# Kernel tuning notes

Measured on AMD Instinct MI355X. Metric: run time of the kernel, lower is better.

The kernel has to match this reference:

```python
import jax, jax.numpy as jnp
import numpy as np

B, DIM, H, W = 4, 256, 64, 64
DSTATE, EXPAND, DCONV = 64, 2, 4
DINNER = EXPAND * DIM            # 512
HEADDIM = 64
NHEADS = DINNER // HEADDIM       # 8
DINPROJ = 2 * DINNER + 2 * DSTATE + NHEADS   # z, xBC, dt
CONVDIM = DINNER + 2 * DSTATE
EPS = 1e-5


def setup_inputs() -> dict:
    key = jax.random.key(0)
    ks = jax.random.split(key, 12)
    n = lambda i, shape, sc=1.0: jax.random.normal(ks[i], shape, jnp.float32) * sc
    return {
        "x": n(0, (B, DIM, H, W)),
        "Q1": n(1, (B, 1, H, W)),
        "Q2": n(2, (B, 1, H, W)),
        "S": jax.random.uniform(ks[3], (B, 1, H, W), jnp.float32),
        "ln_g": jnp.ones((DIM,), jnp.float32),
        "ln_b": jnp.zeros((DIM,), jnp.float32),
        "W_in": n(4, (DIM, DINPROJ), 0.02),
        "conv_w": n(5, (CONVDIM, DCONV), 0.2),
        "conv_b": jnp.zeros((CONVDIM,), jnp.float32),
        "dt_bias": n(6, (NHEADS,), 0.5),
        "A_log": jnp.log(jnp.linspace(1.0, 8.0, NHEADS)).astype(jnp.float32),
        "Dskip": n(7, (NHEADS,), 0.3) + 1.0,
        "norm_w": jnp.ones((DINNER,), jnp.float32),
        "W_out": n(8, (DINNER, DIM), 0.02),
        "gn_g": jnp.ones((DIM,), jnp.float32),
        "gn_b": jnp.zeros((DIM,), jnp.float32),
        "conv1_w": n(9, (DIM, DIM), 0.05),
    }


def _mamba(seq, W_in, conv_w, conv_b, dt_bias, A_log, Dskip, norm_w, W_out):
    # seq: (Ns, L, D) -- Mamba-2 style SSD forward
    Ns, L, _ = seq.shape
    zxbcdt = seq @ W_in                                   # (Ns,L,DINPROJ)
    z = zxbcdt[..., :DINNER]
    xBC = zxbcdt[..., DINNER:DINNER + CONVDIM]
    dt = zxbcdt[..., DINNER + CONVDIM:]                   # (Ns,L,nh)
    # causal depthwise conv (kernel DCONV) + silu
    xp = jnp.pad(xBC, ((0, 0), (DCONV - 1, 0), (0, 0)))
    xBC = sum(conv_w[:, k] * xp[:, k:k + L, :] for k in range(DCONV)) + conv_b
    xBC = jax.nn.silu(xBC)
    xh = xBC[..., :DINNER].reshape(Ns, L, NHEADS, HEADDIM)
    Bm = xBC[..., DINNER:DINNER + DSTATE]                 # (Ns,L,n) ngroups=1
    Cm = xBC[..., DINNER + DSTATE:]
    dt = jax.nn.softplus(dt + dt_bias)
    A = -jnp.exp(A_log)                                   # (nh,)
    dA = jnp.exp(dt * A)                                  # (Ns,L,nh)
    dBx = jnp.einsum('slh,slhp,sln->slhpn', dt, xh, Bm)   # (Ns,L,nh,hd,n)

    def step(h, inp):
        a, bx, c = inp
        h = a[:, :, None, None] * h + bx                  # (Ns,nh,hd,n)
        return h, jnp.einsum('shpn,sn->shp', h, c)

    h0 = jnp.zeros((Ns, NHEADS, HEADDIM, DSTATE), seq.dtype)
    _, ys = jax.lax.scan(step, h0, (dA.transpose(1, 0, 2),
                                    dBx.transpose(1, 0, 2, 3, 4),
                                    Cm.transpose(1, 0, 2)))
    y = ys.transpose(1, 0, 2, 3) + Dskip[None, None, :, None] * xh
    y = y.reshape(Ns, L, DINNER)
    y = y * jax.nn.silu(z)                                # gated RMSNorm
    y = y * jax.lax.rsqrt(jnp.mean(y * y, axis=-1, keepdims=True) + EPS) * norm_w
    return y @ W_out


def _scan_merge(xn, dim_scan, mp):
    Bb, C, Hh, Ww = xn.shape
    if dim_scan == 3:
        seq = xn.transpose(0, 2, 3, 1).reshape(Bb * Hh, Ww, C)
    else:
        seq = xn.transpose(0, 3, 2, 1).reshape(Bb * Ww, Hh, C)
    fwd = _mamba(seq, *mp)
    bwd = jnp.flip(_mamba(jnp.flip(seq, 1), *mp), 1)
    out = 0.5 * (fwd + bwd)
    if dim_scan == 3:
        return out.reshape(Bb, Hh, Ww, C).transpose(0, 3, 1, 2)
    return out.reshape(Bb, Ww, Hh, C).transpose(0, 3, 2, 1)


def reference(x, Q1, Q2, S, ln_g, ln_b, W_in, conv_w, conv_b, dt_bias, A_log,
              Dskip, norm_w, W_out, gn_g, gn_b, conv1_w):
    # LayerNorm over channel dim
    xt = x.transpose(0, 2, 3, 1)                          # (B,H,W,C)
    mu = xt.mean(-1, keepdims=True)
    var = ((xt - mu) ** 2).mean(-1, keepdims=True)
    xn = ((xt - mu) * jax.lax.rsqrt(var + EPS) * ln_g + ln_b).transpose(0, 3, 1, 2)
    mp = (W_in, conv_w, conv_b, dt_bias, A_log, Dskip, norm_w, W_out)
    f_H = _scan_merge(xn, 3, mp)                          # horizontal (along W)
    f_V = _scan_merge(xn, 2, mp)                          # vertical (along H)
    alpha = jax.nn.sigmoid(Q1)
    fg = (alpha * f_H + (1 - alpha) * f_V) * (0.5 + 0.5 * S)
    # out_proj: Conv1x1 (no bias) + GroupNorm(1) + GELU
    y = jnp.einsum('bchw,oc->bohw', fg, conv1_w)
    mu = y.mean((1, 2, 3), keepdims=True)
    var = ((y - mu) ** 2).mean((1, 2, 3), keepdims=True)
    y = (y - mu) * jax.lax.rsqrt(var + EPS) * gn_g[None, :, None, None] + gn_b[None, :, None, None]
    return jax.nn.gelu(y, approximate=False)
```

## Files before the change

kernel.cpp:

```cpp
#include <hip/hip_runtime.h>
#include <hip/hip_bf16.h>

#define EPSF 1e-5f

typedef unsigned short u16;
typedef __attribute__((ext_vector_type(8))) short short8;
typedef __attribute__((ext_vector_type(4))) float f32x4;

__device__ __forceinline__ float sigf(float x){ return 1.f/(1.f+__expf(-x)); }
__device__ __forceinline__ float siluf(float x){ return x/(1.f+__expf(-x)); }
__device__ __forceinline__ u16 f2bf(float x){ __hip_bfloat16 h = __float2bfloat16(x); return *reinterpret_cast<u16*>(&h); }
__device__ __forceinline__ float bf2f(u16 u){ __hip_bfloat16 h; *reinterpret_cast<u16*>(&h) = u; return __bfloat162float(h); }

union BF8 { short8 v; u16 h[8]; uint4 q; };

__device__ __forceinline__ short8 ldg_frag(const u16* p){
  BF8 u; u.q = *(const uint4*)p; return u.v;
}
#define MFMA16(a,b,c) __builtin_amdgcn_mfma_f32_16x16x32_bf16((a),(b),(c),0,0,0)

__global__ __launch_bounds__(256) void k_ln(const float* __restrict__ x,
                                            const float* __restrict__ g,
                                            const float* __restrict__ b,
                                            u16* __restrict__ xn){
  __shared__ float XL[256][65];
  __shared__ float red[2][4][64];
  __shared__ float muL[64], rsL[64];
  int blk = blockIdx.x; int bb = blk>>6, h = blk&63;
  int t = threadIdx.x;
  const float* xb = x + ((size_t)bb*256*4096) + h*64;
  for(int i=0;i<64;i++){ int idx = t + 256*i; int c = idx>>6, w = idx&63;
    XL[c][w] = xb[(size_t)c*4096 + w]; }
  __syncthreads();
  { int w = t & 63, q = t >> 6;
    float s1=0, s2=0;
    for(int c=q*64;c<q*64+64;c++){ float v = XL[c][w]; s1+=v; s2+=v*v; }
    red[0][q][w]=s1; red[1][q][w]=s2; }
  __syncthreads();
  if(t<64){ float a=0,c2=0;
    for(int q=0;q<4;q++){a+=red[0][q][t]; c2+=red[1][q][t];}
    float mu=a*(1.f/256.f); float var=c2*(1.f/256.f)-mu*mu;
    muL[t]=mu; rsL[t]=rsqrtf(var+EPSF); }
  __syncthreads();
  u16* xnb = xn + (size_t)(bb*64+h)*64*256;
  for(int i=0;i<64;i++){ int idx = t + 256*i; int w = idx>>8, c = idx&255;
    float v = (XL[c][w]-muL[w])*rsL[w]*g[c]+b[c];
    xnb[w*256 + c] = f2bf(v); }
}

__global__ __launch_bounds__(256) void k_prep(const float* __restrict__ Wi,
                                              u16* __restrict__ WiF,
                                              const float* __restrict__ Wo,
                                              const float* __restrict__ W1,
                                              u16* __restrict__ WCF){
  __shared__ float WoL[256];
  int blk = blockIdx.x;
  int t = threadIdx.x;
  if(blk < 146){
    int f = blk*256 + t;
    int lane = f & 63, kk = (f>>6)&7, ji = f>>9;
    int g = lane>>4, c16 = lane&15;
    int j = ji*16 + c16;
    BF8 o;
    #pragma unroll
    for(int i=0;i<8;i++){
      int k = kk*32 + g*8 + i;
      o.h[i] = (j < 1160) ? f2bf(Wi[(size_t)k*1160 + j]) : (u16)0;
    }
    *(uint4*)(WiF + (size_t)f*8) = o.q;
  } else {
    int k = blk - 146;
    int o = t;
    WoL[o] = Wo[(size_t)k*256 + o];
    __syncthreads();
    const float4* w1p = (const float4*)(W1 + (size_t)o*256);
    const float4* wop = (const float4*)WoL;
    float d = 0.f;
    #pragma unroll 8
    for(int i=0;i<64;i++){
      float4 a = wop[i]; float4 b = w1p[i];
      d += a.x*b.x + a.y*b.y + a.z*b.z + a.w*b.w;
    }
    int kk = k>>5, g = (k>>3)&3, i2 = k&7;
    int ci = o>>4, c16 = o&15;
    WCF[(size_t)((((ci*16+kk)*4+g)*16+c16)*8 + i2)] = f2bf(d);
  }
}

__global__ __launch_bounds__(512, 4) void k_gemm_in(const u16* __restrict__ xn,
    const u16* __restrict__ WiF, const float* __restrict__ dtb,
    const float* __restrict__ alog,
    u16* __restrict__ zg, u16* __restrict__ xbc,
    float* __restrict__ dtp, float* __restrict__ dtA){
  __shared__ u16 XL[64][264];
  int id = blockIdx.x;
  int xcd = id & 7;
  int rem = id >> 3;
  int rb_local = rem / 5;
  int cb = rem - rb_local*5;
  int rb = xcd*32 + rb_local;
  int t = threadIdx.x;
  int w = t>>6, lane = t&63, g = lane>>4, c16 = lane&15;

  const u16* asrc = xn + (size_t)rb*64*256;
  #pragma unroll
  for(int i=0;i<4;i++){
    int idx = t + 512*i;
    int row = idx>>5, ch = idx&31;
    *(uint4*)&XL[row][ch*8] = *(const uint4*)(asrc + (size_t)row*256 + ch*8);
  }
  __syncthreads();

  int jbase = cb*15;
  int jcount = (cb==4) ? 13 : 15;
  int jl0 = w*2;

  f32x4 acc[2][4];
  #pragma unroll
  for(int jj=0;jj<2;jj++){
    #pragma unroll
    for(int li=0;li<4;li++) acc[jj][li] = (f32x4){0.f,0.f,0.f,0.f};
  }
  #pragma unroll
  for(int kk=0;kk<8;++kk){
    short8 a0 = *(const short8*)&XL[ 0 + c16][kk*32+g*8];
    short8 a1 = *(const short8*)&XL[16 + c16][kk*32+g*8];
    short8 a2 = *(const short8*)&XL[32 + c16][kk*32+g*8];
    short8 a3 = *(const short8*)&XL[48 + c16][kk*32+g*8];
    #pragma unroll
    for(int jj=0;jj<2;++jj){
      if(jl0+jj < jcount){
        int ji = jbase + jl0 + jj;
        short8 bf = ldg_frag(WiF + ((size_t)(ji*8+kk)*64 + lane)*8);
        acc[jj][0] = MFMA16(a0, bf, acc[jj][0]);
        acc[jj][1] = MFMA16(a1, bf, acc[jj][1]);
        acc[jj][2] = MFMA16(a2, bf, acc[jj][2]);
        acc[jj][3] = MFMA16(a3, bf, acc[jj][3]);
      }
    }
  }
  int mbase = rb*64;
  #pragma unroll
  for(int jj=0;jj<2;++jj){
    if(jl0+jj >= jcount) continue;
    int ji = jbase + jl0 + jj;
    if(ji < 32){
      int col = ji*16 + c16;
      #pragma unroll
      for(int li=0;li<4;li++){
        #pragma unroll
        for(int r2=0;r2<4;r2++)
          zg[(size_t)(mbase + li*16 + g*4 + r2)*512 + col] = f2bf(siluf(acc[jj][li][r2]));
      }
    } else if(ji < 72){
      int col = ji*16 + c16 - 512;
      #pragma unroll
      for(int li=0;li<4;li++){
        #pragma unroll
        for(int r2=0;r2<4;r2++)
          xbc[(size_t)(mbase + li*16 + g*4 + r2)*640 + col] = f2bf(acc[jj][li][r2]);
      }
    } else if(c16 < 8){
      int hd = c16;
      float A = -expf(alog[hd]);
      float bias = dtb[hd];
      #pragma unroll
      for(int li=0;li<4;li++){
        #pragma unroll
        for(int r2=0;r2<4;r2++){
          int m = mbase + li*16 + g*4 + r2;
          float v = acc[jj][li][r2] + bias;
          float sp = (v>20.f)? v : log1pf(expf(v));
          dtp[(size_t)((m>>6)*8 + hd)*64 + (m&63)] = sp;
          dtA[(size_t)((m>>6)*8 + hd)*64 + (m&63)] = sp*A;
        }
      }
    }
  }
}

__global__ __launch_bounds__(512) void k_convBC(const u16* __restrict__ xbc,
    const float* __restrict__ convw, const float* __restrict__ convb,
    u16* __restrict__ bH0, u16* __restrict__ bH1,
    u16* __restrict__ bV0, u16* __restrict__ bV1){
  int s = blockIdx.x, y = blockIdx.y;
  int dirb = y&1, dirV = y>>1;
  int t = threadIdx.x;
  int u = t>>3, cg = t&7;
  int b_ = s>>6, r_ = s&63;
  int cB = 512 + cg*8, cC = 576 + cg*8;
  float4 cwB[8], cwC[8]; float cbB[8], cbC[8];
  #pragma unroll
  for(int i=0;i<8;i++){
    cwB[i] = *(const float4*)(convw + (size_t)(cB+i)*4);
    cwC[i] = *(const float4*)(convw + (size_t)(cC+i)*4);
    cbB[i] = convb[cB+i]; cbC[i] = convb[cC+i];
  }
  BF8 wB[4], wC[4];
  #pragma unroll
  for(int j=0;j<4;j++){
    int p = u - 3 + j;
    if(p >= 0){
      int m = dirb ? 63-p : p;
      size_t row = dirV ? ((size_t)b_*4096 + (size_t)m*64 + r_) : ((size_t)s*64 + m);
      wB[j].q = *(const uint4*)(xbc + row*640 + cB);
      wC[j].q = *(const uint4*)(xbc + row*640 + cC);
    } else { wB[j].q = (uint4){0u,0u,0u,0u}; wC[j].q = (uint4){0u,0u,0u,0u}; }
  }
  BF8 oB, oC;
  #pragma unroll
  for(int ch=0; ch<8; ++ch){
    float vB = cbB[ch] + cwB[ch].w*bf2f(wB[3].h[ch]) + cwB[ch].z*bf2f(wB[2].h[ch])
                       + cwB[ch].y*bf2f(wB[1].h[ch]) + cwB[ch].x*bf2f(wB[0].h[ch]);
    float vC = cbC[ch] + cwC[ch].w*bf2f(wC[3].h[ch]) + cwC[ch].z*bf2f(wC[2].h[ch])
                       + cwC[ch].y*bf2f(wC[1].h[ch]) + cwC[ch].x*bf2f(wC[0].h[ch]);
    oB.h[ch] = f2bf(siluf(vB));
    oC.h[ch] = f2bf(siluf(vC));
  }
  u16* dst = ((y==0)? bH0 : (y==1)? bH1 : (y==2)? bV0 : bV1) + ((size_t)(s*64+u))*128;
  *(uint4*)(dst + cg*8)      = oB.q;
  *(uint4*)(dst + 64 + cg*8) = oC.q;
}

__global__ __launch_bounds__(512, 4) void k_scan4(
    const u16* __restrict__ xbc,
    const u16* __restrict__ bH0, const u16* __restrict__ bH1,
    const u16* __restrict__ bV0, const u16* __restrict__ bV1,
    const float* __restrict__ convw, const float* __restrict__ convb,
    const float* __restrict__ dtp_g, const float* __restrict__ dtA_g,
    const float* __restrict__ dskip,
    u16* __restrict__ UH0, u16* __restrict__ UH1,
    u16* __restrict__ UV0, u16* __restrict__ UV1){
  __shared__ __align__(16) char smem[78976];
  u16 (*XV)[520] = (u16(*)[520])smem;
  float* Gtri = (float*)(smem + 66560);
  float* sL   = (float*)(smem + 74880);
  float* dtL  = (float*)(smem + 76928);

  int id = blockIdx.x;
  int xcd = id & 7;
  int rem = id >> 3;
  int s = xcd*32 + (rem>>2);
  int y = rem & 3;
  int t = threadIdx.x;
  int dirb = y&1, dirV = y>>1;
  int w = t>>6, lane = t&63, g = lane>>4, c16 = lane&15;
  int b_ = s>>6, r_ = s&63;
  float dsk = dskip[w];
  const u16* xc = ((y==0)? bH0 : (y==1)? bH1 : (y==2)? bV0 : bV1) + (size_t)s*64*128;
  u16* un = ((y==0)? UH0 : (y==1)? UH1 : (y==2)? UV0 : UV1) + (size_t)s*64*512;

  {
    int tt = dirb ? 63-lane : lane;
    size_t dti = dirV ? ((size_t)((b_*64 + tt)*8 + w))*64 + r_
                      : ((size_t)(s*8 + w))*64 + tt;
    float a = dtA_g[dti];
    float d = dtp_g[dti];
    #pragma unroll
    for(int off=1; off<64; off<<=1){
      float nb = __shfl_up(a, off, 64);
      if(lane >= off) a += nb;
    }
    sL[w*64+lane] = a;
    dtL[w*64+lane] = d;
  }
  #pragma unroll
  for(int tt2=0; tt2<2; ++tt2){
    int tile = 2*w + tt2, li = tile>>2, ji = tile&3;
    f32x4 acc = {0.f,0.f,0.f,0.f};
    #pragma unroll
    for(int kk=0; kk<2; ++kk){
      short8 af = ldg_frag(xc + (size_t)(li*16 + c16)*128 + 64 + kk*32 + g*8);
      short8 bf = ldg_frag(xc + (size_t)(ji*16 + c16)*128 +      kk*32 + g*8);
      acc = MFMA16(af, bf, acc);
    }
    int col = ji*16 + c16;
    #pragma unroll
    for(int r=0;r<4;r++){
      int row = li*16 + g*4 + r;
      if(col <= row) Gtri[(row*(row+1))/2 + col] = acc[r];
    }
  }
  int c0 = lane*8;
  #pragma unroll
  for(int it=0; it<8; ++it){
    int tr = w + 8*it;
    int m = dirb ? 63-tr : tr;
    size_t row = dirV ? ((size_t)b_*4096 + (size_t)m*64 + r_) : ((size_t)s*64 + m);
    *(uint4*)&XV[tr][c0] = *(const uint4*)(xbc + row*640 + c0);
  }
  __syncthreads();
  {
    float4 cwx[8]; float cbx[8];
    #pragma unroll
    for(int i=0;i<8;i++){
      cwx[i] = *(const float4*)(convw + (size_t)(c0+i)*4);
      cbx[i] = convb[c0+i];
    }
    BF8 outr[8];
    #pragma unroll
    for(int it=0; it<8; ++it){
      int tr = w + 8*it;
      BF8 wnd[4];
      #pragma unroll
      for(int j=0;j<4;j++){
        int p = tr - 3 + j;
        if(p >= 0) wnd[j].q = *(const uint4*)&XV[p][c0];
        else       wnd[j].q = (uint4){0u,0u,0u,0u};
      }
      #pragma unroll
      for(int ch=0; ch<8; ++ch){
        float v = cbx[ch] + cwx[ch].w*bf2f(wnd[3].h[ch]) + cwx[ch].z*bf2f(wnd[2].h[ch])
                          + cwx[ch].y*bf2f(wnd[1].h[ch]) + cwx[ch].x*bf2f(wnd[0].h[ch]);
        outr[it].h[ch] = f2bf(siluf(v));
      }
    }
    __syncthreads();
    #pragma unroll
    for(int it=0; it<8; ++it)
      *(uint4*)&XV[w + 8*it][c0] = outr[it].q;
  }
  __syncthreads();
  short8 xfr[4][2];
  #pragma unroll
  for(int pi=0; pi<4; ++pi){
    #pragma unroll
    for(int kk=0; kk<2; ++kk){
      BF8 u;
      #pragma unroll
      for(int i=0;i<8;i++){
        int uu = kk*32 + g*8 + i;
        u.h[i] = XV[uu][w*64 + pi*16 + c16];
      }
      xfr[pi][kk] = u.v;
    }
  }
  #pragma unroll 1
  for(int li=0; li<4; ++li){
    int tr = li*16 + c16;
    float sl = sL[w*64 + tr];
    int tb = (tr*(tr+1))/2;
    short8 mfr[2];
    #pragma unroll
    for(int kk=0; kk<2; ++kk){
      BF8 u;
      #pragma unroll
      for(int i=0;i<8;i++){
        int uu = kk*32 + g*8 + i;
        float m = 0.f;
        if(uu <= tr){
          m = __expf(sl - sL[w*64+uu]) * dtL[w*64+uu] * Gtri[tb + uu];
          if(uu == tr) m += dsk;
        }
        u.h[i] = f2bf(m);
      }
      mfr[kk] = u.v;
    }
    #pragma unroll
    for(int pi=0; pi<4; ++pi){
      f32x4 acc = {0.f,0.f,0.f,0.f};
      acc = MFMA16(mfr[0], xfr[pi][0], acc);
      acc = MFMA16(mfr[1], xfr[pi][1], acc);
      #pragma unroll
      for(int r=0;r<4;r++){
        int trow = li*16 + g*4 + r;
        int lorig = dirb ? 63-trow : trow;
        XV[lorig][w*64 + pi*16 + c16] = f2bf(acc[r]);
      }
    }
  }
  __syncthreads();
  #pragma unroll
  for(int rr=0; rr<8; ++rr){
    int l = w*8 + rr;
    *(uint4*)(un + (size_t)l*512 + lane*8) = *(const uint4*)&XV[l][lane*8];
  }
}

__global__ __launch_bounds__(1024, 4) void k_blendfinal(
    const u16* __restrict__ UH0, const u16* __restrict__ UH1,
    const u16* __restrict__ UV0, const u16* __restrict__ UV1,
    const u16* __restrict__ zg, const float* __restrict__ normw,
    const float* __restrict__ Q1, const float* __restrict__ Sx,
    const u16* __restrict__ WCF,
    float* __restrict__ out, float* __restrict__ stats){
  __shared__ u16 A[64][520];
  __shared__ float asL[64], bsL[64];
  __shared__ float nwL[512];
  __shared__ float red[2][16];
  int blk = blockIdx.x; int bb = blk>>6, h = blk&63;
  int t = threadIdx.x;
  if(t<64){
    float qv = Q1[bb*4096 + h*64 + t];
    float sv = Sx[bb*4096 + h*64 + t];
    float al = sigf(qv);
    float sc = 0.5f + 0.5f*sv;
    asL[t] = al*sc; bsL[t] = (1.f-al)*sc;
  }
  if(t < 512) nwL[t] = normw[t];
  __syncthreads();
  int wv = t>>6, lane = t&63, g = lane>>4, c16 = lane&15;
  #pragma unroll 1
  for(int i=0;i<4;i++){
    int wp = wv + 16*i;
    int c8 = lane*8;
    size_t rH = ((size_t)((bb*64+h)*64 + wp))*512 + c8;
    size_t rV = ((size_t)((bb*64+wp)*64 + h))*512 + c8;
    BF8 h0,h1,v0,v1,z8;
    h0.q = *(const uint4*)(UH0 + rH);
    h1.q = *(const uint4*)(UH1 + rH);
    v0.q = *(const uint4*)(UV0 + rV);
    v1.q = *(const uint4*)(UV1 + rV);
    z8.q = *(const uint4*)(zg  + rH);
    float gh0[8], gh1[8], gv0[8], gv1[8];
    float sh0=0.f, sh1=0.f, sv0=0.f, sv1=0.f;
    #pragma unroll
    for(int j=0;j<8;j++){
      float zv = bf2f(z8.h[j]);
      gh0[j] = bf2f(h0.h[j])*zv; sh0 += gh0[j]*gh0[j];
      gh1[j] = bf2f(h1.h[j])*zv; sh1 += gh1[j]*gh1[j];
      gv0[j] = bf2f(v0.h[j])*zv; sv0 += gv0[j]*gv0[j];
      gv1[j] = bf2f(v1.h[j])*zv; sv1 += gv1[j]*gv1[j];
    }
    #pragma unroll
    for(int off=32; off>=1; off>>=1){
      sh0 += __shfl_xor(sh0, off, 64); sh1 += __shfl_xor(sh1, off, 64);
      sv0 += __shfl_xor(sv0, off, 64); sv1 += __shfl_xor(sv1, off, 64);
    }
    float rh0 = rsqrtf(sh0*(1.f/512.f)+EPSF);
    float rh1 = rsqrtf(sh1*(1.f/512.f)+EPSF);
    float rv0 = rsqrtf(sv0*(1.f/512.f)+EPSF);
    float rv1 = rsqrtf(sv1*(1.f/512.f)+EPSF);
    float aw = 0.5f*asL[wp], bw = 0.5f*bsL[wp];
    BF8 o;
    #pragma unroll
    for(int j=0;j<8;j++){
      float u = nwL[c8+j]*(aw*(gh0[j]*rh0 + gh1[j]*rh1) + bw*(gv0[j]*rv0 + gv1[j]*rv1));
      o.h[j] = f2bf(u);
    }
    *(uint4*)&A[wp][c8] = o.q;
  }
  __syncthreads();
  int ci = wv;
  f32x4 acc0={0.f,0.f,0.f,0.f}, acc1=acc0, acc2=acc0, acc3=acc0;
  #pragma unroll 2
  for(int kk=0; kk<16; ++kk){
    short8 bfr = ldg_frag(WCF + (size_t)((((ci*16+kk)*4+g)*16+c16)*8));
    short8 a0 = *(const short8*)&A[ 0+c16][kk*32+g*8];
    short8 a1 = *(const short8*)&A[16+c16][kk*32+g*8];
    short8 a2 = *(const short8*)&A[32+c16][kk*32+g*8];
    short8 a3 = *(const short8*)&A[48+c16][kk*32+g*8];
    acc0 = MFMA16(a0,bfr,acc0); acc1 = MFMA16(a1,bfr,acc1);
    acc2 = MFMA16(a2,bfr,acc2); acc3 = MFMA16(a3,bfr,acc3);
  }
  float s1=0.f, s2=0.f;
  int o_ = ci*16 + c16;
  #pragma unroll
  for(int li=0; li<4; ++li){
    f32x4 a = (li==0)?acc0 : (li==1)?acc1 : (li==2)?acc2 : acc3;
    int w0 = li*16 + g*4;
    float4 vv = {a[0], a[1], a[2], a[3]};
    s1 += (vv.x+vv.y)+(vv.z+vv.w);
    s2 += (vv.x*vv.x+vv.y*vv.y)+(vv.z*vv.z+vv.w*vv.w);
    *(float4*)(out + (((size_t)(bb*256+o_)*64 + h)*64 + w0)) = vv;
  }
  #pragma unroll
  for(int off=32;off>=1;off>>=1){ s1+=__shfl_xor(s1,off,64); s2+=__shfl_xor(s2,off,64); }
  if(lane==0){ red[0][wv]=s1; red[1][wv]=s2; }
  __syncthreads();
  if(t==0){
    float a=0.f,b=0.f;
    #pragma unroll
    for(int i=0;i<16;i++){ a+=red[0][i]; b+=red[1][i]; }
    stats[blk*2+0]=a; stats[blk*2+1]=b;
  }
}

__global__ __launch_bounds__(256) void k_final(float* __restrict__ out,
    const float* __restrict__ stats, const float* __restrict__ gg,
    const float* __restrict__ gb){
  __shared__ float red[64][2];
  __shared__ float mv[2];
  int blk = blockIdx.x; int bb = blk>>6, h = blk&63;
  int t = threadIdx.x;
  if(t<64){ red[t][0] = stats[(bb*64+t)*2+0]; red[t][1] = stats[(bb*64+t)*2+1]; }
  __syncthreads();
  if(t==0){
    float s1=0.f,s2=0.f;
    for(int i=0;i<64;i++){ s1+=red[i][0]; s2+=red[i][1]; }
    float mu = s1*(1.f/1048576.f);
    float var = s2*(1.f/1048576.f) - mu*mu;
    mv[0]=mu; mv[1]=rsqrtf(var+EPSF);
  }
  __syncthreads();
  float mu = mv[0], rs = mv[1];
  for(int i=0;i<64;i++){ int idx=t+256*i; int o=idx>>6, w=idx&63;
    size_t gidx = (size_t)((bb*256+o)*64+h)*64+w;
    float v = out[gidx];
    float yn = (v-mu)*rs*gg[o] + gb[o];
    out[gidx] = 0.5f*yn*(1.f+erff(yn*0.70710678118654752f));
  }
}

extern "C" void kernel_launch(void* const* d_in, const int* in_sizes, int n_in,
                              void* d_out, int out_size, void* d_ws, size_t ws_size,
                              hipStream_t stream) {
  const float* x     = (const float*)d_in[0];
  const float* Q1    = (const float*)d_in[1];
  const float* Sx    = (const float*)d_in[3];
  const float* lng   = (const float*)d_in[4];
  const float* lnb   = (const float*)d_in[5];
  const float* Wi    = (const float*)d_in[6];
  const float* convw = (const float*)d_in[7];
  const float* convb = (const float*)d_in[8];
  const float* dtb   = (const float*)d_in[9];
  const float* alog  = (const float*)d_in[10];
  const float* dskip = (const float*)d_in[11];
  const float* normw = (const float*)d_in[12];
  const float* Wo    = (const float*)d_in[13];
  const float* gg    = (const float*)d_in[14];
  const float* gb    = (const float*)d_in[15];
  const float* W1    = (const float*)d_in[16];
  float* out = (float*)d_out;
  char* ws = (char*)d_ws;

  size_t o = 0;
  u16*   xnb  = (u16*)(ws + o);  o += (size_t)16384*256*2;
  u16*   zgb  = (u16*)(ws + o);  o += (size_t)16384*512*2;
  u16*   xbc  = (u16*)(ws + o);  o += (size_t)16384*640*2;
  u16*   bH0  = (u16*)(ws + o);  o += (size_t)16384*128*2;
  u16*   bH1  = (u16*)(ws + o);  o += (size_t)16384*128*2;
  u16*   bV0  = (u16*)(ws + o);  o += (size_t)16384*128*2;
  u16*   bV1  = (u16*)(ws + o);  o += (size_t)16384*128*2;
  u16*   UH0  = (u16*)(ws + o);  o += (size_t)16384*512*2;
  u16*   UH1  = (u16*)(ws + o);  o += (size_t)16384*512*2;
  u16*   UV0  = (u16*)(ws + o);  o += (size_t)16384*512*2;
  u16*   UV1  = (u16*)(ws + o);  o += (size_t)16384*512*2;
  float* dtp  = (float*)(ws + o); o += (size_t)131072*4;
  float* dtA  = (float*)(ws + o); o += (size_t)131072*4;
  float* stats= (float*)(ws + o); o += 4096;
  u16*   WiF  = (u16*)(ws + o);  o += (size_t)73*8*64*8*2;
  u16*   WCF  = (u16*)(ws + o);  o += (size_t)16384*8*2;

  k_ln<<<256, 256, 0, stream>>>(x, lng, lnb, xnb);
  k_prep<<<658, 256, 0, stream>>>(Wi, WiF, Wo, W1, WCF);
  k_gemm_in<<<1280, 512, 0, stream>>>(xnb, WiF, dtb, alog,
                                      zgb, xbc, dtp, dtA);
  k_convBC<<<dim3(256,4), 512, 0, stream>>>(xbc, convw, convb, bH0, bH1, bV0, bV1);
  k_scan4<<<1024, 512, 0, stream>>>(xbc, bH0, bH1, bV0, bV1, convw, convb,
                                    dtp, dtA, dskip, UH0, UH1, UV0, UV1);
  k_blendfinal<<<256, 1024, 0, stream>>>(UH0, UH1, UV0, UV1, zgb, normw,
                                         Q1, Sx, WCF, out, stats);
  k_final<<<256, 256, 0, stream>>>(out, stats, gg, gb);
}
```

Before: 169.0 us.

## Fuse both scan directions and gated RMSNorm into scan kernel

The scan kernel now handles the forward and reverse directions of one sequence in a single block and applies the z-gating and RMSNorm inside the kernel. It sums the two normalized directions into one buffer per orientation, so it writes two intermediate buffers instead of four. This cuts global writes and the later reads in the blend kernel, which now does only the alpha/S-weighted blend. In exchange the grid is halved to 512 blocks with occupancy hint 2, so each block runs the two directions one after the other and has less parallelism; the partial sum is also kept in bf16 between passes.

```diff
diff --git a/kernel.cpp b/kernel.cpp
--- a/kernel.cpp
+++ b/kernel.cpp
@@ -222,171 +222,196 @@
   *(uint4*)(dst + 64 + cg*8) = oC.q;
 }
 
-__global__ __launch_bounds__(512, 4) void k_scan4(
+__global__ __launch_bounds__(512, 2) void k_scan2(
     const u16* __restrict__ xbc,
     const u16* __restrict__ bH0, const u16* __restrict__ bH1,
     const u16* __restrict__ bV0, const u16* __restrict__ bV1,
+    const u16* __restrict__ zg,
     const float* __restrict__ convw, const float* __restrict__ convb,
     const float* __restrict__ dtp_g, const float* __restrict__ dtA_g,
-    const float* __restrict__ dskip,
-    u16* __restrict__ UH0, u16* __restrict__ UH1,
-    u16* __restrict__ UV0, u16* __restrict__ UV1){
-  __shared__ __align__(16) char smem[78976];
+    const float* __restrict__ dskip, const float* __restrict__ normw,
+    u16* __restrict__ UHs, u16* __restrict__ UVs){
+  __shared__ __align__(16) char smem[81024];
   u16 (*XV)[520] = (u16(*)[520])smem;
   float* Gtri = (float*)(smem + 66560);
   float* sL   = (float*)(smem + 74880);
   float* dtL  = (float*)(smem + 76928);
+  float* nwL  = (float*)(smem + 78976);
 
   int id = blockIdx.x;
   int xcd = id & 7;
   int rem = id >> 3;
-  int s = xcd*32 + (rem>>2);
-  int y = rem & 3;
-  int t = threadIdx.x;
-  int dirb = y&1, dirV = y>>1;
+  int s = xcd*32 + (rem>>1);
+  int dirV = rem & 1;
+  int t = threadIdx.x;
   int w = t>>6, lane = t&63, g = lane>>4, c16 = lane&15;
   int b_ = s>>6, r_ = s&63;
   float dsk = dskip[w];
-  const u16* xc = ((y==0)? bH0 : (y==1)? bH1 : (y==2)? bV0 : bV1) + (size_t)s*64*128;
-  u16* un = ((y==0)? UH0 : (y==1)? UH1 : (y==2)? UV0 : UV1) + (size_t)s*64*512;
-
-  {
-    int tt = dirb ? 63-lane : lane;
-    size_t dti = dirV ? ((size_t)((b_*64 + tt)*8 + w))*64 + r_
-                      : ((size_t)(s*8 + w))*64 + tt;
-    float a = dtA_g[dti];
-    float d = dtp_g[dti];
-    #pragma unroll
-    for(int off=1; off<64; off<<=1){
-      float nb = __shfl_up(a, off, 64);
-      if(lane >= off) a += nb;
-    }
-    sL[w*64+lane] = a;
-    dtL[w*64+lane] = d;
-  }
-  #pragma unroll
-  for(int tt2=0; tt2<2; ++tt2){
-    int tile = 2*w + tt2, li = tile>>2, ji = tile&3;
-    f32x4 acc = {0.f,0.f,0.f,0.f};
-    #pragma unroll
-    for(int kk=0; kk<2; ++kk){
-      short8 af = ldg_frag(xc + (size_t)(li*16 + c16)*128 + 64 + kk*32 + g*8);
-      short8 bf = ldg_frag(xc + (size_t)(ji*16 + c16)*128 +      kk*32 + g*8);
-      acc = MFMA16(af, bf, acc);
-    }
-    int col = ji*16 + c16;
-    #pragma unroll
-    for(int r=0;r<4;r++){
-      int row = li*16 + g*4 + r;
-      if(col <= row) Gtri[(row*(row+1))/2 + col] = acc[r];
-    }
-  }
   int c0 = lane*8;
-  #pragma unroll
-  for(int it=0; it<8; ++it){
-    int tr = w + 8*it;
-    int m = dirb ? 63-tr : tr;
-    size_t row = dirV ? ((size_t)b_*4096 + (size_t)m*64 + r_) : ((size_t)s*64 + m);
-    *(uint4*)&XV[tr][c0] = *(const uint4*)(xbc + row*640 + c0);
-  }
-  __syncthreads();
-  {
-    float4 cwx[8]; float cbx[8];
-    #pragma unroll
-    for(int i=0;i<8;i++){
-      cwx[i] = *(const float4*)(convw + (size_t)(c0+i)*4);
-      cbx[i] = convb[c0+i];
-    }
-    BF8 outr[8];
+  nwL[t] = normw[t];
+  BF8 uacc[8];
+
+  #pragma unroll 1
+  for(int dirb=0; dirb<2; ++dirb){
+    __syncthreads();
+    const u16* xc = (dirV ? (dirb? bV1 : bV0) : (dirb? bH1 : bH0)) + (size_t)s*64*128;
+    {
+      int tt = dirb ? 63-lane : lane;
+      size_t dti = dirV ? ((size_t)((b_*64 + tt)*8 + w))*64 + r_
+                        : ((size_t)(s*8 + w))*64 + tt;
+      float a = dtA_g[dti];
+      float d = dtp_g[dti];
+      #pragma unroll
+      for(int off=1; off<64; off<<=1){
+        float nb = __shfl_up(a, off, 64);
+        if(lane >= off) a += nb;
+      }
+      sL[w*64+lane] = a;
+      dtL[w*64+lane] = d;
+    }
+    #pragma unroll
+    for(int tt2=0; tt2<2; ++tt2){
+      int tile = 2*w + tt2, li = tile>>2, ji = tile&3;
+      f32x4 acc = {0.f,0.f,0.f,0.f};
+      #pragma unroll
+      for(int kk=0; kk<2; ++kk){
+        short8 af = ldg_frag(xc + (size_t)(li*16 + c16)*128 + 64 + kk*32 + g*8);
+        short8 bf = ldg_frag(xc + (size_t)(ji*16 + c16)*128 +      kk*32 + g*8);
+        acc = MFMA16(af, bf, acc);
+      }
+      int col = ji*16 + c16;
+      #pragma unroll
+      for(int r=0;r<4;r++){
+        int row = li*16 + g*4 + r;
+        if(col <= row) Gtri[(row*(row+1))/2 + col] = acc[r];
+      }
+    }
     #pragma unroll
     for(int it=0; it<8; ++it){
       int tr = w + 8*it;
-      BF8 wnd[4];
-      #pragma unroll
-      for(int j=0;j<4;j++){
-        int p = tr - 3 + j;
-        if(p >= 0) wnd[j].q = *(const uint4*)&XV[p][c0];
-        else       wnd[j].q = (uint4){0u,0u,0u,0u};
-      }
-      #pragma unroll
-      for(int ch=0; ch<8; ++ch){
-        float v = cbx[ch] + cwx[ch].w*bf2f(wnd[3].h[ch]) + cwx[ch].z*bf2f(wnd[2].h[ch])
-                          + cwx[ch].y*bf2f(wnd[1].h[ch]) + cwx[ch].x*bf2f(wnd[0].h[ch]);
-        outr[it].h[ch] = f2bf(siluf(v));
-      }
+      int m = dirb ? 63-tr : tr;
+      size_t row = dirV ? ((size_t)b_*4096 + (size_t)m*64 + r_) : ((size_t)s*64 + m);
+      *(uint4*)&XV[tr][c0] = *(const uint4*)(xbc + row*640 + c0);
     }
     __syncthreads();
-    #pragma unroll
-    for(int it=0; it<8; ++it)
-      *(uint4*)&XV[w + 8*it][c0] = outr[it].q;
-  }
-  __syncthreads();
-  short8 xfr[4][2];
-  #pragma unroll
-  for(int pi=0; pi<4; ++pi){
-    #pragma unroll
-    for(int kk=0; kk<2; ++kk){
-      BF8 u;
+    {
+      float4 cwx[8]; float cbx[8];
       #pragma unroll
       for(int i=0;i<8;i++){
-        int uu = kk*32 + g*8 + i;
-        u.h[i] = XV[uu][w*64 + pi*16 + c16];
-      }
-      xfr[pi][kk] = u.v;
-    }
-  }
-  #pragma unroll 1
-  for(int li=0; li<4; ++li){
-    int tr = li*16 + c16;
-    float sl = sL[w*64 + tr];
-    int tb = (tr*(tr+1))/2;
-    short8 mfr[2];
-    #pragma unroll
-    for(int kk=0; kk<2; ++kk){
-      BF8 u;
-      #pragma unroll
-      for(int i=0;i<8;i++){
-        int uu = kk*32 + g*8 + i;
-        float m = 0.f;
-        if(uu <= tr){
-          m = __expf(sl - sL[w*64+uu]) * dtL[w*64+uu] * Gtri[tb + uu];
-          if(uu == tr) m += dsk;
+        cwx[i] = *(const float4*)(convw + (size_t)(c0+i)*4);
+        cbx[i] = convb[c0+i];
+      }
+      BF8 outr[8];
+      #pragma unroll
+      for(int it=0; it<8; ++it){
+        int tr = w + 8*it;
+        BF8 wnd[4];
+        #pragma unroll
+        for(int j=0;j<4;j++){
+          int p = tr - 3 + j;
+          if(p >= 0) wnd[j].q = *(const uint4*)&XV[p][c0];
+          else       wnd[j].q = (uint4){0u,0u,0u,0u};
         }
-        u.h[i] = f2bf(m);
-      }
-      mfr[kk] = u.v;
-    }
+        #pragma unroll
+        for(int ch=0; ch<8; ++ch){
+          float v = cbx[ch] + cwx[ch].w*bf2f(wnd[3].h[ch]) + cwx[ch].z*bf2f(wnd[2].h[ch])
+                            + cwx[ch].y*bf2f(wnd[1].h[ch]) + cwx[ch].x*bf2f(wnd[0].h[ch]);
+          outr[it].h[ch] = f2bf(siluf(v));
+        }
+      }
+      __syncthreads();
+      #pragma unroll
+      for(int it=0; it<8; ++it)
+        *(uint4*)&XV[w + 8*it][c0] = outr[it].q;
+    }
+    __syncthreads();
+    short8 xfr[4][2];
     #pragma unroll
     for(int pi=0; pi<4; ++pi){
-      f32x4 acc = {0.f,0.f,0.f,0.f};
-      acc = MFMA16(mfr[0], xfr[pi][0], acc);
-      acc = MFMA16(mfr[1], xfr[pi][1], acc);
-      #pragma unroll
-      for(int r=0;r<4;r++){
-        int trow = li*16 + g*4 + r;
-        int lorig = dirb ? 63-trow : trow;
-        XV[lorig][w*64 + pi*16 + c16] = f2bf(acc[r]);
-      }
-    }
-  }
-  __syncthreads();
+      #pragma unroll
+      for(int kk=0; kk<2; ++kk){
+        BF8 u;
+        #pragma unroll
+        for(int i=0;i<8;i++){
+          int uu = kk*32 + g*8 + i;
+          u.h[i] = XV[uu][w*64 + pi*16 + c16];
+        }
+        xfr[pi][kk] = u.v;
+      }
+    }
+    #pragma unroll 1
+    for(int li=0; li<4; ++li){
+      int tr = li*16 + c16;
+      float sl = sL[w*64 + tr];
+      int tb = (tr*(tr+1))/2;
+      short8 mfr[2];
+      #pragma unroll
+      for(int kk=0; kk<2; ++kk){
+        BF8 u;
+        #pragma unroll
+        for(int i=0;i<8;i++){
+          int uu = kk*32 + g*8 + i;
+          float m = 0.f;
+          if(uu <= tr){
+            m = __expf(sl - sL[w*64+uu]) * dtL[w*64+uu] * Gtri[tb + uu];
+            if(uu == tr) m += dsk;
+          }
+          u.h[i] = f2bf(m);
+        }
+        mfr[kk] = u.v;
+      }
+      #pragma unroll
+      for(int pi=0; pi<4; ++pi){
+        f32x4 acc = {0.f,0.f,0.f,0.f};
+        acc = MFMA16(mfr[0], xfr[pi][0], acc);
+        acc = MFMA16(mfr[1], xfr[pi][1], acc);
+        #pragma unroll
+        for(int r=0;r<4;r++){
+          int trow = li*16 + g*4 + r;
+          int lorig = dirb ? 63-trow : trow;
+          XV[lorig][w*64 + pi*16 + c16] = f2bf(acc[r]);
+        }
+      }
+    }
+    __syncthreads();
+    #pragma unroll 1
+    for(int rr=0; rr<8; ++rr){
+      int l = w*8 + rr;
+      size_t zrow = dirV ? ((size_t)b_*4096 + (size_t)l*64 + r_) : ((size_t)s*64 + l);
+      BF8 yv, z8;
+      yv.q = *(const uint4*)&XV[l][c0];
+      z8.q = *(const uint4*)(zg + zrow*512 + c0);
+      float gv[8]; float ss = 0.f;
+      #pragma unroll
+      for(int i=0;i<8;i++){ gv[i] = bf2f(yv.h[i]) * bf2f(z8.h[i]); ss += gv[i]*gv[i]; }
+      #pragma unroll
+      for(int off=32; off>=1; off>>=1) ss += __shfl_xor(ss, off, 64);
+      float rs = rsqrtf(ss*(1.f/512.f) + EPSF);
+      if(dirb==0){
+        #pragma unroll
+        for(int i=0;i<8;i++) uacc[rr].h[i] = f2bf(0.5f*gv[i]*rs*nwL[c0+i]);
+      } else {
+        #pragma unroll
+        for(int i=0;i<8;i++)
+          uacc[rr].h[i] = f2bf(bf2f(uacc[rr].h[i]) + 0.5f*gv[i]*rs*nwL[c0+i]);
+      }
+    }
+  }
+  u16* un = (dirV ? UVs : UHs) + (size_t)s*64*512;
   #pragma unroll
   for(int rr=0; rr<8; ++rr){
     int l = w*8 + rr;
-    *(uint4*)(un + (size_t)l*512 + lane*8) = *(const uint4*)&XV[l][lane*8];
+    *(uint4*)(un + (size_t)l*512 + c0) = uacc[rr].q;
   }
 }
 
 __global__ __launch_bounds__(1024, 4) void k_blendfinal(
-    const u16* __restrict__ UH0, const u16* __restrict__ UH1,
-    const u16* __restrict__ UV0, const u16* __restrict__ UV1,
-    const u16* __restrict__ zg, const float* __restrict__ normw,
+    const u16* __restrict__ UHs, const u16* __restrict__ UVs,
     const float* __restrict__ Q1, const float* __restrict__ Sx,
     const u16* __restrict__ WCF,
     float* __restrict__ out, float* __restrict__ stats){
   __shared__ u16 A[64][520];
   __shared__ float asL[64], bsL[64];
-  __shared__ float nwL[512];
   __shared__ float red[2][16];
   int blk = blockIdx.x; int bb = blk>>6, h = blk&63;
   int t = threadIdx.x;
@@ -397,47 +422,21 @@
     float sc = 0.5f + 0.5f*sv;
     asL[t] = al*sc; bsL[t] = (1.f-al)*sc;
   }
-  if(t < 512) nwL[t] = normw[t];
   __syncthreads();
   int wv = t>>6, lane = t&63, g = lane>>4, c16 = lane&15;
-  #pragma unroll 1
+  #pragma unroll
   for(int i=0;i<4;i++){
     int wp = wv + 16*i;
     int c8 = lane*8;
     size_t rH = ((size_t)((bb*64+h)*64 + wp))*512 + c8;
     size_t rV = ((size_t)((bb*64+wp)*64 + h))*512 + c8;
-    BF8 h0,h1,v0,v1,z8;
-    h0.q = *(const uint4*)(UH0 + rH);
-    h1.q = *(const uint4*)(UH1 + rH);
-    v0.q = *(const uint4*)(UV0 + rV);
-    v1.q = *(const uint4*)(UV1 + rV);
-    z8.q = *(const uint4*)(zg  + rH);
-    float gh0[8], gh1[8], gv0[8], gv1[8];
-    float sh0=0.f, sh1=0.f, sv0=0.f, sv1=0.f;
-    #pragma unroll
-    for(int j=0;j<8;j++){
-      float zv = bf2f(z8.h[j]);
-      gh0[j] = bf2f(h0.h[j])*zv; sh0 += gh0[j]*gh0[j];
-      gh1[j] = bf2f(h1.h[j])*zv; sh1 += gh1[j]*gh1[j];
-      gv0[j] = bf2f(v0.h[j])*zv; sv0 += gv0[j]*gv0[j];
-      gv1[j] = bf2f(v1.h[j])*zv; sv1 += gv1[j]*gv1[j];
-    }
-    #pragma unroll
-    for(int off=32; off>=1; off>>=1){
-      sh0 += __shfl_xor(sh0, off, 64); sh1 += __shfl_xor(sh1, off, 64);
-      sv0 += __shfl_xor(sv0, off, 64); sv1 += __shfl_xor(sv1, off, 64);
-    }
-    float rh0 = rsqrtf(sh0*(1.f/512.f)+EPSF);
-    float rh1 = rsqrtf(sh1*(1.f/512.f)+EPSF);
-    float rv0 = rsqrtf(sv0*(1.f/512.f)+EPSF);
-    float rv1 = rsqrtf(sv1*(1.f/512.f)+EPSF);
-    float aw = 0.5f*asL[wp], bw = 0.5f*bsL[wp];
-    BF8 o;
-    #pragma unroll
-    for(int j=0;j<8;j++){
-      float u = nwL[c8+j]*(aw*(gh0[j]*rh0 + gh1[j]*rh1) + bw*(gv0[j]*rv0 + gv1[j]*rv1));
-      o.h[j] = f2bf(u);
-    }
+    BF8 uh, uv, o;
+    uh.q = *(const uint4*)(UHs + rH);
+    uv.q = *(const uint4*)(UVs + rV);
+    float aw = asL[wp], bw = bsL[wp];
+    #pragma unroll
+    for(int j=0;j<8;j++)
+      o.h[j] = f2bf(aw*bf2f(uh.h[j]) + bw*bf2f(uv.h[j]));
     *(uint4*)&A[wp][c8] = o.q;
   }
   __syncthreads();
@@ -532,10 +531,8 @@
   u16*   bH1  = (u16*)(ws + o);  o += (size_t)16384*128*2;
   u16*   bV0  = (u16*)(ws + o);  o += (size_t)16384*128*2;
   u16*   bV1  = (u16*)(ws + o);  o += (size_t)16384*128*2;
-  u16*   UH0  = (u16*)(ws + o);  o += (size_t)16384*512*2;
-  u16*   UH1  = (u16*)(ws + o);  o += (size_t)16384*512*2;
-  u16*   UV0  = (u16*)(ws + o);  o += (size_t)16384*512*2;
-  u16*   UV1  = (u16*)(ws + o);  o += (size_t)16384*512*2;
+  u16*   UHs  = (u16*)(ws + o);  o += (size_t)16384*512*2;
+  u16*   UVs  = (u16*)(ws + o);  o += (size_t)16384*512*2;
   float* dtp  = (float*)(ws + o); o += (size_t)131072*4;
   float* dtA  = (float*)(ws + o); o += (size_t)131072*4;
   float* stats= (float*)(ws + o); o += 4096;
@@ -547,9 +544,8 @@
   k_gemm_in<<<1280, 512, 0, stream>>>(xnb, WiF, dtb, alog,
                                       zgb, xbc, dtp, dtA);
   k_convBC<<<dim3(256,4), 512, 0, stream>>>(xbc, convw, convb, bH0, bH1, bV0, bV1);
-  k_scan4<<<1024, 512, 0, stream>>>(xbc, bH0, bH1, bV0, bV1, convw, convb,
-                                    dtp, dtA, dskip, UH0, UH1, UV0, UV1);
-  k_blendfinal<<<256, 1024, 0, stream>>>(UH0, UH1, UV0, UV1, zgb, normw,
-                                         Q1, Sx, WCF, out, stats);
+  k_scan2<<<512, 512, 0, stream>>>(xbc, bH0, bH1, bV0, bV1, zgb, convw, convb,
+                                   dtp, dtA, dskip, normw, UHs, UVs);
+  k_blendfinal<<<256, 1024, 0, stream>>>(UHs, UVs, Q1, Sx, WCF, out, stats);
   k_final<<<256, 256, 0, stream>>>(out, stats, gg, gb);
 }
```

After: 208.8 us (median of 2 runs). 23.6% more time.
